# Performance work log

Measured on AMD Instinct MI355X. Metric: run time of the kernel, lower is better.

Reference implementation:

```python
import jax, jax.numpy as jnp
import numpy as np

LN_EPS = 1e-5

def _layernorm(x, g, b):
    mu = jnp.mean(x, axis=-1, keepdims=True)
    var = jnp.var(x, axis=-1, keepdims=True)
    return (x - mu) * jax.lax.rsqrt(var + LN_EPS) * g + b

def setup_inputs() -> dict:
    key = jax.random.key(0)
    B, S, D, H = 2, 2048, 1024, 16
    dh = D // H          # 64
    r = 48               # r_attn = int(0.75*min(D,dh))
    r_out = 768          # int(0.75*D)
    I = 4 * D            # GPT-2 MLP inner dim
    r_mlp = 512          # int(0.5*min(D,I))
    ks = jax.random.split(key, 24)
    sc = lambda *sh: 0.02
    inp = {
        'hidden_states': jax.random.normal(ks[0], (B, S, D), jnp.float32),
        'ln1_g': jnp.ones((D,), jnp.float32), 'ln1_b': jnp.zeros((D,), jnp.float32),
        'ln2_g': jnp.ones((D,), jnp.float32), 'ln2_b': jnp.zeros((D,), jnp.float32),
        'q_U': jax.random.normal(ks[1], (D, H, r), jnp.float32) * 0.02,
        'q_V': jax.random.normal(ks[2], (H, r, dh), jnp.float32) * 0.02,
        'q_b': jax.random.normal(ks[3], (H, dh), jnp.float32) * 0.02,
        'k_U': jax.random.normal(ks[4], (D, H, r), jnp.float32) * 0.02,
        'k_V': jax.random.normal(ks[5], (H, r, dh), jnp.float32) * 0.02,
        'k_b': jax.random.normal(ks[6], (H, dh), jnp.float32) * 0.02,
        'v_U': jax.random.normal(ks[7], (D, H, r), jnp.float32) * 0.02,
        'v_V': jax.random.normal(ks[8], (H, r, dh), jnp.float32) * 0.02,
        'v_b': jax.random.normal(ks[9], (H, dh), jnp.float32) * 0.02,
        'out_U': jax.random.normal(ks[10], (D, r_out), jnp.float32) * 0.02,
        'out_V': jax.random.normal(ks[11], (r_out, D), jnp.float32) * 0.02,
        'out_b': jnp.zeros((D,), jnp.float32),
        'fc1_U': jax.random.normal(ks[12], (D, r_mlp), jnp.float32) * 0.02,
        'fc1_V': jax.random.normal(ks[13], (r_mlp, I), jnp.float32) * 0.02,
        'fc1_b': jnp.zeros((I,), jnp.float32),
        'fc2_U': jax.random.normal(ks[14], (I, r_mlp), jnp.float32) * 0.02,
        'fc2_V': jax.random.normal(ks[15], (r_mlp, D), jnp.float32) * 0.02,
        'fc2_b': jnp.zeros((D,), jnp.float32),
    }
    return inp

def reference(hidden_states, ln1_g, ln1_b, ln2_g, ln2_b,
              q_U, q_V, q_b, k_U, k_V, k_b, v_U, v_V, v_b,
              out_U, out_V, out_b, fc1_U, fc1_V, fc1_b, fc2_U, fc2_V, fc2_b):
    B, S, D = hidden_states.shape
    H, dh = q_V.shape[0], q_V.shape[2]
    x = _layernorm(hidden_states, ln1_g, ln1_b)
    # low-rank per-head projections (latent P then reconstruct)
    Q = jnp.einsum('bsd,dhr,hre->bhse', x, q_U, q_V) + q_b[None, :, None, :]
    Pk = jnp.einsum('bsd,dhr->bhsr', x, k_U)
    Pv = jnp.einsum('bsd,dhr->bhsr', x, v_U)
    K = jnp.einsum('bhsr,hrd->bhsd', Pk, k_V) + k_b[None, :, None, :]
    V = jnp.einsum('bhsr,hrd->bhsd', Pv, v_V) + v_b[None, :, None, :]
    # causal scaled dot-product attention
    scale = 1.0 / jnp.sqrt(jnp.asarray(dh, x.dtype))
    scores = jnp.einsum('bhse,bhte->bhst', Q, K) * scale
    causal = jnp.tril(jnp.ones((S, S), bool))
    scores = jnp.where(causal[None, None], scores, jnp.asarray(-1e9, scores.dtype))
    attn = jax.nn.softmax(scores, axis=-1)
    ctx = jnp.einsum('bhst,bhtd->bhsd', attn, V)          # [B,H,S,dh]
    ctx = ctx.transpose(0, 2, 1, 3).reshape(B, S, D)
    attn_out = (ctx @ out_U) @ out_V + out_b
    h = hidden_states + attn_out
    # low-rank MLP with GPT-2 gelu (tanh approx)
    x2 = _layernorm(h, ln2_g, ln2_b)
    hmid = jax.nn.gelu((x2 @ fc1_U) @ fc1_V + fc1_b, approximate=True)
    mlp_out = (hmid @ fc2_U) @ fc2_V + fc2_b
    return h + mlp_out
```

## Files before the change

kernel.cpp:

```cpp
#include <hip/hip_runtime.h>
#include <hip/hip_bf16.h>

typedef float f32x4 __attribute__((ext_vector_type(4)));
typedef __bf16 bf16x8 __attribute__((ext_vector_type(8)));
typedef __bf16 bf16x4 __attribute__((ext_vector_type(4)));
typedef unsigned short u16x8 __attribute__((ext_vector_type(8)));
typedef unsigned short u16x4 __attribute__((ext_vector_type(4)));

#define QSCALE 0.180336881f

__device__ __forceinline__ unsigned short f2bf(float f) {
  union { float f; unsigned int u; } v; v.f = f;
  return (unsigned short)((v.u + 0x7FFFu + ((v.u >> 16) & 1u)) >> 16);
}

__device__ __forceinline__ f32x4 mfma16(bf16x8 a, bf16x8 b, f32x4 c) {
  return __builtin_amdgcn_mfma_f32_16x16x32_bf16(a, b, c, 0, 0, 0);
}

__device__ __forceinline__ void gload16(const unsigned short* g, unsigned short* l) {
  __builtin_amdgcn_global_load_lds(
      (const __attribute__((address_space(1))) void*)g,
      (__attribute__((address_space(3))) void*)l, 16, 0, 0);
}


__global__ void concat_bias_k(const float* __restrict__ qb, const float* __restrict__ kb,
                              const float* __restrict__ vb, float* __restrict__ out) {
  const int i = blockIdx.x * 256 + threadIdx.x;
  if (i >= 3072) return;
  const float* s = (i < 1024) ? qb : (i < 2048 ? kb : vb);
  out[i] = s[i & 1023] * (i < 1024 ? QSCALE : 1.0f);
}

__global__ void tcvt_k(const float* __restrict__ in, unsigned short* __restrict__ out,
                       int R, int C) {
  __shared__ float tile[32][33];
  const int x = blockIdx.x * 32 + threadIdx.x;
  const int y0 = blockIdx.y * 32;
#pragma unroll
  for (int i = 0; i < 32; i += 8)
    tile[threadIdx.y + i][threadIdx.x] = in[(size_t)(y0 + threadIdx.y + i) * C + x];
  __syncthreads();
  const int ox = y0 + threadIdx.x;
  const int oy0 = blockIdx.x * 32;
#pragma unroll
  for (int i = 0; i < 32; i += 8)
    out[(size_t)(oy0 + threadIdx.y + i) * R + ox] = f2bf(tile[threadIdx.x][threadIdx.y + i]);
}

__global__ void cvt_k(const float* __restrict__ in, unsigned short* __restrict__ out, int n) {
  const int i = (blockIdx.x * 256 + threadIdx.x) * 4;
  if (i >= n) return;
  const f32x4 v = *(const f32x4*)(in + i);
  u16x4 o;
#pragma unroll
  for (int k = 0; k < 4; ++k) o[k] = f2bf(v[k]);
  *(u16x4*)(out + i) = o;
}

__global__ void vtr_k(const unsigned short* __restrict__ QKV, unsigned short* __restrict__ VT) {
  __shared__ unsigned short tile[32][33];
  const int bh = blockIdx.z, b = bh >> 4, h = bh & 15;
  const int s0 = blockIdx.x * 32, d0 = blockIdx.y * 32;
  const unsigned short* src = QKV + (size_t)b * 2048 * 3072 + 2048 + h * 64;
#pragma unroll
  for (int i = 0; i < 32; i += 8)
    tile[threadIdx.y + i][threadIdx.x] = src[(size_t)(s0 + threadIdx.y + i) * 3072 + d0 + threadIdx.x];
  __syncthreads();
  unsigned short* dst = VT + (size_t)bh * 64 * 2048;
#pragma unroll
  for (int i = 0; i < 32; i += 8)
    dst[(size_t)(d0 + threadIdx.y + i) * 2048 + s0 + threadIdx.x] = tile[threadIdx.x][threadIdx.y + i];
}

__global__ __launch_bounds__(256) void wqkv_pre_k(
    const float* __restrict__ qU, const float* __restrict__ qV,
    const float* __restrict__ kU, const float* __restrict__ kV,
    const float* __restrict__ vU, const float* __restrict__ vV,
    unsigned short* __restrict__ WT) {
  __shared__ float Us[64][48];
  __shared__ float Vs[48][64];
  const int m = blockIdx.y >> 4, h = blockIdx.y & 15;
  const int d0 = blockIdx.x * 64;
  const float* U = (m == 0) ? qU : (m == 1 ? kU : vU);
  const float* V = (m == 0) ? qV : (m == 1 ? kV : vV);
  const float qs = (m == 0) ? QSCALE : 1.0f;
  const int t = threadIdx.x;
  for (int idx = t; idx < 64 * 48; idx += 256) {
    const int d = idx / 48, r = idx - d * 48;
    Us[d][r] = U[(size_t)(d0 + d) * 768 + h * 48 + r];
  }
  for (int idx = t; idx < 48 * 64; idx += 256) {
    const int r = idx >> 6, e = idx & 63;
    Vs[r][e] = V[(h * 48 + r) * 64 + e];
  }
  __syncthreads();
  const int e = t & 63, dg = t >> 6;
  for (int j = 0; j < 16; ++j) {
    const int d = dg * 16 + j;
    float s = 0.f;
#pragma unroll
    for (int r = 0; r < 48; ++r) s = fmaf(Us[d][r], Vs[r][e], s);
    WT[(size_t)(m * 1024 + h * 64 + e) * 1024 + d0 + d] = f2bf(s * qs);
  }
}

__global__ __launch_bounds__(256) void ln_k(
    const float* __restrict__ in, const float* __restrict__ gw,
    const float* __restrict__ bw, unsigned short* __restrict__ out) {
  const int row = blockIdx.x, t = threadIdx.x;
  const f32x4 v = *(const f32x4*)(in + (size_t)row * 1024 + t * 4);
  float s = v[0] + v[1] + v[2] + v[3];
  float ss = v[0] * v[0] + v[1] * v[1] + v[2] * v[2] + v[3] * v[3];
#pragma unroll
  for (int off = 1; off < 64; off <<= 1) {
    s += __shfl_xor(s, off);
    ss += __shfl_xor(ss, off);
  }
  __shared__ float red[8];
  if ((t & 63) == 0) { red[(t >> 6) * 2] = s; red[(t >> 6) * 2 + 1] = ss; }
  __syncthreads();
  s = red[0] + red[2] + red[4] + red[6];
  ss = red[1] + red[3] + red[5] + red[7];
  const float mean = s * (1.0f / 1024.0f);
  const float rstd = rsqrtf(ss * (1.0f / 1024.0f) - mean * mean + 1e-5f);
  const f32x4 g4 = *(const f32x4*)(gw + t * 4);
  const f32x4 b4 = *(const f32x4*)(bw + t * 4);
  u16x4 o;
#pragma unroll
  for (int i = 0; i < 4; ++i) o[i] = f2bf((v[i] - mean) * rstd * g4[i] + b4[i]);
  *(u16x4*)(out + (size_t)row * 1024 + t * 4) = o;
}

__device__ __forceinline__ void xcd_swz(int& bx, int& by, int nx, int ny) {
  const int nwg = nx * ny;
  if ((nwg & 7) == 0) {
    const int d = by * nx + bx;
    const int k = (d & 7) * (nwg >> 3) + (d >> 3);
    bx = k % nx;
    by = k / nx;
  }
}

template <int BM, int BN, int EPI, int OUTBF>
__global__ __launch_bounds__(256) void gemm_k(
    const unsigned short* __restrict__ A, const unsigned short* __restrict__ Bt,
    const float* __restrict__ bias, const float* __restrict__ resid,
    void* __restrict__ Cout, int M, int N, int K) {
  constexpr int MI = BM / 32;
  constexpr int FN = BN / 32;
  __shared__ unsigned short As[2][BM * 32];
  __shared__ unsigned short Bs[2][BN * 32];
  int bxi = blockIdx.x, byi = blockIdx.y;
  xcd_swz(bxi, byi, gridDim.x, gridDim.y);
  const int t = threadIdx.x;
  const int lane = t & 63, wid = t >> 6;
  const int m0 = byi * BM, n0 = bxi * BN;
  const int wm = (wid >> 1) * (BM / 2), wn = (wid & 1) * (BN / 2);
  const int fr = lane & 15, fg = (lane >> 4) * 8;

  f32x4 acc[MI][FN];
#pragma unroll
  for (int i = 0; i < MI; ++i)
#pragma unroll
    for (int j = 0; j < FN; ++j) acc[i][j] = (f32x4){0.f, 0.f, 0.f, 0.f};

  const unsigned short* Ag0 = A + (size_t)(m0 + (t >> 2)) * K + (t & 3) * 8;
  const unsigned short* Ag1 = A + (size_t)(m0 + 64 + (t >> 2)) * K + (t & 3) * 8;
  const unsigned short* Bg0 = Bt + (size_t)(n0 + (t >> 2)) * K + (t & 3) * 8;
  const unsigned short* Bg1 = Bt + (size_t)(n0 + 64 + (t >> 2)) * K + (t & 3) * 8;
  const int l0 = t * 8;

#define GEMM_STAGE(buf, ke)                                   \
  {                                                           \
    gload16(Ag0 + (ke), &As[buf][l0]);                        \
    if (BM == 128) gload16(Ag1 + (ke), &As[buf][l0 + 2048]);  \
    gload16(Bg0 + (ke), &Bs[buf][l0]);                        \
    if (BN == 128) gload16(Bg1 + (ke), &Bs[buf][l0 + 2048]);  \
  }

  const int nk = K >> 5;
  GEMM_STAGE(0, 0);

  for (int kt = 0; kt < nk; ++kt) {
    const int cur = kt & 1;
    __syncthreads();
    if (kt + 1 < nk) GEMM_STAGE(cur ^ 1, (kt + 1) * 32);
    bf16x8 af[MI], bfr[FN];
#pragma unroll
    for (int i = 0; i < MI; ++i) af[i] = *(const bf16x8*)&As[cur][(wm + i * 16 + fr) * 32 + fg];
#pragma unroll
    for (int j = 0; j < FN; ++j) bfr[j] = *(const bf16x8*)&Bs[cur][(wn + j * 16 + fr) * 32 + fg];
#pragma unroll
    for (int i = 0; i < MI; ++i)
#pragma unroll
      for (int j = 0; j < FN; ++j) acc[i][j] = mfma16(af[i], bfr[j], acc[i][j]);
  }
#undef GEMM_STAGE

#pragma unroll
  for (int j = 0; j < FN; ++j) {
    const int col = n0 + wn + j * 16 + fr;
    const float bval = (EPI >= 1) ? bias[col] : 0.0f;
#pragma unroll
    for (int i = 0; i < MI; ++i) {
#pragma unroll
      for (int r = 0; r < 4; ++r) {
        const int row = m0 + wm + i * 16 + ((lane >> 4) << 2) + r;
        float v = acc[i][j][r] + bval;
        if (EPI == 2) {
          const float z = 0.7978845608028654f * (v + 0.044715f * v * v * v);
          v = v - v / (__expf(2.0f * z) + 1.0f);
        }
        if (EPI == 3) v += resid[(size_t)row * N + col];
        if (OUTBF)
          ((unsigned short*)Cout)[(size_t)row * N + col] = f2bf(v);
        else
          ((float*)Cout)[(size_t)row * N + col] = v;
      }
    }
  }
}

__global__ __launch_bounds__(512) void attn_k(
    const unsigned short* __restrict__ QKV, const unsigned short* __restrict__ VT,
    unsigned short* __restrict__ ctx) {
  __shared__ unsigned short Ks[2][64 * 64];
  __shared__ unsigned short Vs[2][64 * 64];
  __shared__ unsigned short Ps[8][16 * 64];
  int bxi = blockIdx.x, byi = blockIdx.y;
  xcd_swz(bxi, byi, 16, 32);
  const int qi = ((byi >> 1) & 1) ? (15 - bxi) : bxi;
  const int bh = byi, b = bh >> 4, h = bh & 15;
  const int nt = 2 * qi + 2;
  const int q0b = qi * 128;
  const int t = threadIdx.x, lane = t & 63, w = t >> 6;
  const int g = lane >> 4, c = lane & 15;
  const int cks = c & 7;
  const size_t base = (size_t)b * 2048 * 3072;

  const int r0 = t >> 3, ch0 = t & 7;
  const int lw = r0 * 64 + ((ch0 ^ (r0 & 7)) * 8);
  const unsigned short* Kg = QKV + base + 1024 + h * 64 + (size_t)r0 * 3072 + ch0 * 8;
  const unsigned short* Vg = VT + ((size_t)bh * 64 + r0) * 2048 + ch0 * 8;

  const int kro0 = (g ^ cks) * 8, kro1 = ((4 + g) ^ cks) * 8;

  bf16x8 onef;
#pragma unroll
  for (int i = 0; i < 8; ++i) onef[i] = (__bf16)1.0f;

  const int qrow = q0b + w * 16 + c;
  const unsigned short* qp = QKV + base + (size_t)qrow * 3072 + h * 64 + g * 8;
  const bf16x8 qf0 = *(const bf16x8*)qp;
  const bf16x8 qf1 = *(const bf16x8*)(qp + 32);

  f32x4 o[4];
#pragma unroll
  for (int d = 0; d < 4; ++d) o[d] = (f32x4){0.f, 0.f, 0.f, 0.f};
  f32x4 ol = (f32x4){0.f, 0.f, 0.f, 0.f};
  float mrow = -1e30f;

  u16x8 kr, vr;
#define ATTN_LOAD(kt_)                                        \
  {                                                           \
    kr = *(const u16x8*)(Kg + (size_t)(kt_) * 64 * 3072);     \
    vr = *(const u16x8*)(Vg + (kt_) * 64);                    \
  }
#define ATTN_WRITE(buf)                                       \
  {                                                           \
    *(u16x8*)&Ks[buf][lw] = kr;                               \
    *(u16x8*)&Vs[buf][lw] = vr;                               \
  }

  ATTN_LOAD(0);
  ATTN_WRITE(0);
  if (nt > 1) ATTN_LOAD(1);
  __syncthreads();

  const int fsrc = g * 20;

  for (int j = 0; j < nt; ++j) {
    const int cur = j & 1;
    const int kbase = j * 64;
    const bool active = (kbase <= q0b + w * 16 + 15);

    if (active) {
      f32x4 s4[4];
      __builtin_amdgcn_s_setprio(1);
#pragma unroll
      for (int t16 = 0; t16 < 4; ++t16) {
        const int krow = (t16 * 16 + c) * 64;
        const bf16x8 kf0 = *(const bf16x8*)&Ks[cur][krow + kro0];
        const bf16x8 kf1 = *(const bf16x8*)&Ks[cur][krow + kro1];
        f32x4 a = (f32x4){0.f, 0.f, 0.f, 0.f};
        a = mfma16(kf0, qf0, a);
        a = mfma16(kf1, qf1, a);
        s4[t16] = a;
      }
      __builtin_amdgcn_s_setprio(0);
      if (kbase + 63 > qrow) {
#pragma unroll
        for (int t16 = 0; t16 < 4; ++t16)
#pragma unroll
          for (int r = 0; r < 4; ++r)
            if (kbase + t16 * 16 + 4 * g + r > qrow) s4[t16][r] = -1e30f;
      }
      float mx = s4[0][0];
#pragma unroll
      for (int t16 = 0; t16 < 4; ++t16)
#pragma unroll
        for (int r = 0; r < 4; ++r) mx = fmaxf(mx, s4[t16][r]);
      mx = fmaxf(mx, __shfl_xor(mx, 16));
      mx = fmaxf(mx, __shfl_xor(mx, 32));
      const float mn = fmaxf(mrow, mx);
      const float fac = exp2f(mrow - mn);
      mrow = mn;
#pragma unroll
      for (int t16 = 0; t16 < 4; ++t16) {
        bf16x4 pw;
#pragma unroll
        for (int r = 0; r < 4; ++r) pw[r] = (__bf16)exp2f(s4[t16][r] - mrow);
        *(bf16x4*)&Ps[w][c * 64 + (((2 * t16 + (g >> 1)) ^ cks) * 8) + (g & 1) * 4] = pw;
      }
      float fo[4];
#pragma unroll
      for (int r = 0; r < 4; ++r) fo[r] = __shfl(fac, fsrc + r);
#pragma unroll
      for (int d = 0; d < 4; ++d)
#pragma unroll
        for (int r = 0; r < 4; ++r) o[d][r] *= fo[r];
#pragma unroll
      for (int r = 0; r < 4; ++r) ol[r] *= fo[r];
      __builtin_amdgcn_s_setprio(1);
#pragma unroll
      for (int ks = 0; ks < 2; ++ks) {
        const int po = ((ks * 4 + g) ^ cks) * 8;
        const bf16x8 pf = *(const bf16x8*)&Ps[w][c * 64 + po];
#pragma unroll
        for (int d = 0; d < 4; ++d) {
          const bf16x8 vf = *(const bf16x8*)&Vs[cur][(d * 16 + c) * 64 + po];
          o[d] = mfma16(pf, vf, o[d]);
        }
        ol = mfma16(pf, onef, ol);
      }
      __builtin_amdgcn_s_setprio(0);
    }

    if (j + 1 < nt) {
      __syncthreads();
      ATTN_WRITE(cur ^ 1);
      if (j + 2 < nt) ATTN_LOAD(j + 2);
      __syncthreads();
    }
  }
#pragma unroll
  for (int d = 0; d < 4; ++d)
#pragma unroll
    for (int r = 0; r < 4; ++r) {
      const float v = o[d][r] / ol[r];
      ctx[(size_t)(b * 2048 + q0b + w * 16 + g * 4 + r) * 1024 + h * 64 + d * 16 + c] = f2bf(v);
    }
#undef ATTN_LOAD
#undef ATTN_WRITE
}


extern "C" void kernel_launch(void* const* d_in, const int* in_sizes, int n_in,
                              void* d_out, int out_size, void* d_ws, size_t ws_size,
                              hipStream_t stream) {
  const float* hidden = (const float*)d_in[0];
  const float* ln1g = (const float*)d_in[1];
  const float* ln1b = (const float*)d_in[2];
  const float* ln2g = (const float*)d_in[3];
  const float* ln2b = (const float*)d_in[4];
  const float* qU = (const float*)d_in[5];
  const float* qV = (const float*)d_in[6];
  const float* qb = (const float*)d_in[7];
  const float* kU = (const float*)d_in[8];
  const float* kV = (const float*)d_in[9];
  const float* kb = (const float*)d_in[10];
  const float* vU = (const float*)d_in[11];
  const float* vV = (const float*)d_in[12];
  const float* vb = (const float*)d_in[13];
  const float* outU = (const float*)d_in[14];
  const float* outV = (const float*)d_in[15];
  const float* outb = (const float*)d_in[16];
  const float* fc1U = (const float*)d_in[17];
  const float* fc1V = (const float*)d_in[18];
  const float* fc1b = (const float*)d_in[19];
  const float* fc2U = (const float*)d_in[20];
  const float* fc2V = (const float*)d_in[21];
  const float* fc2b = (const float*)d_in[22];
  float* out = (float*)d_out;

  char* p = (char*)d_ws;
  unsigned short* x1x2 = (unsigned short*)p; p += (size_t)4096 * 1024 * 2;
  unsigned short* WqT_t1 = (unsigned short*)p; p += (size_t)3072 * 1024 * 2;
  float* bqkv = (float*)p; p += 3072 * 4;
  char* bigA = p; p += (size_t)4096 * 3072 * 2 + (size_t)4096 * 1024 * 2;
  unsigned short* QKV = (unsigned short*)bigA;
  unsigned short* ctxb = (unsigned short*)(bigA + (size_t)4096 * 3072 * 2);
  unsigned short* hmid = (unsigned short*)bigA;
  char* wo = p; p += (size_t)1024 * 768 * 2 * 2 + (size_t)1024 * 1024 * 2;
  unsigned short* outUb = (unsigned short*)wo;
  unsigned short* outVT = (unsigned short*)(wo + (size_t)1024 * 768 * 2);
  unsigned short* WoutT = (unsigned short*)(wo + (size_t)1024 * 768 * 2 * 2);
  unsigned short* t2 = (unsigned short*)wo;
  float* hbuf = (float*)p; p += (size_t)4096 * 1024 * 4;
  unsigned short* VT = (unsigned short*)hbuf;
  unsigned short* fc1UT = (unsigned short*)p; p += (size_t)512 * 1024 * 2;
  unsigned short* fc1VT = (unsigned short*)p; p += (size_t)4096 * 512 * 2;
  unsigned short* fc2UT = (unsigned short*)p; p += (size_t)512 * 4096 * 2;
  unsigned short* fc2VT = (unsigned short*)p; p += (size_t)1024 * 512 * 2;

  const dim3 b256(256);
  const dim3 tb(32, 8);

  concat_bias_k<<<12, b256, 0, stream>>>(qb, kb, vb, bqkv);
  wqkv_pre_k<<<dim3(16, 48), b256, 0, stream>>>(qU, qV, kU, kV, vU, vV, WqT_t1);
  tcvt_k<<<dim3(32, 24), tb, 0, stream>>>(outV, outVT, 768, 1024);
  cvt_k<<<768, b256, 0, stream>>>(outU, outUb, 1024 * 768);
  tcvt_k<<<dim3(16, 32), tb, 0, stream>>>(fc1U, fc1UT, 1024, 512);
  tcvt_k<<<dim3(128, 16), tb, 0, stream>>>(fc1V, fc1VT, 512, 4096);
  tcvt_k<<<dim3(16, 128), tb, 0, stream>>>(fc2U, fc2UT, 4096, 512);
  tcvt_k<<<dim3(32, 16), tb, 0, stream>>>(fc2V, fc2VT, 512, 1024);

  ln_k<<<4096, b256, 0, stream>>>(hidden, ln1g, ln1b, x1x2);
  gemm_k<128, 128, 1, 1><<<dim3(24, 32), b256, 0, stream>>>(x1x2, WqT_t1, bqkv, nullptr, QKV, 4096, 3072, 1024);
  vtr_k<<<dim3(64, 2, 32), tb, 0, stream>>>(QKV, VT);
  gemm_k<128, 128, 0, 1><<<dim3(8, 8), b256, 0, stream>>>(outVT, outUb, nullptr, nullptr, WoutT, 1024, 1024, 768);
  attn_k<<<dim3(16, 32), dim3(512), 0, stream>>>(QKV, VT, ctxb);
  gemm_k<64, 128, 3, 0><<<dim3(8, 64), b256, 0, stream>>>(ctxb, WoutT, outb, hidden, hbuf, 4096, 1024, 1024);

  ln_k<<<4096, b256, 0, stream>>>(hbuf, ln2g, ln2b, x1x2);
  gemm_k<64, 64, 0, 1><<<dim3(8, 64), b256, 0, stream>>>(x1x2, fc1UT, nullptr, nullptr, WqT_t1, 4096, 512, 1024);
  gemm_k<128, 128, 2, 1><<<dim3(32, 32), b256, 0, stream>>>(WqT_t1, fc1VT, fc1b, nullptr, hmid, 4096, 4096, 512);
  gemm_k<64, 64, 0, 1><<<dim3(8, 64), b256, 0, stream>>>(hmid, fc2UT, nullptr, nullptr, t2, 4096, 512, 4096);
  gemm_k<64, 128, 3, 0><<<dim3(8, 64), b256, 0, stream>>>(t2, fc2VT, fc2b, hbuf, out, 4096, 1024, 512);
}
```

Before: 291.4 us.

## Triple-buffer GEMM k-loop with vmcnt waits and stage bf16 epilogue through LDS

Moves the GEMM main loop from double to triple buffering. It prefetches two stages ahead and uses explicit s_waitcnt vmcnt plus a raw barrier instead of __syncthreads, so global loads overlap more with MFMA work. For bf16 outputs, each wave writes its results into a padded LDS tile and then stores 16-byte vectors per row, replacing scattered 2-byte global stores. The cost is more LDS per block, which may lower occupancy, and the hand-tuned wait counts depend on how many loads each stage issues.

```diff
diff --git a/kernel.cpp b/kernel.cpp
--- a/kernel.cpp
+++ b/kernel.cpp
@@ -150,8 +150,13 @@
     void* __restrict__ Cout, int M, int N, int K) {
   constexpr int MI = BM / 32;
   constexpr int FN = BN / 32;
-  __shared__ unsigned short As[2][BM * 32];
-  __shared__ unsigned short Bs[2][BN * 32];
+  constexpr int NL = (BM == 128 ? 2 : 1) + (BN == 128 ? 2 : 1);
+  constexpr int SM_KLOOP = 3 * (BM + BN) * 32;
+  constexpr int SM_EPI = OUTBF ? 4 * (BM / 2) * 72 : 0;
+  constexpr int SME = SM_KLOOP > SM_EPI ? SM_KLOOP : SM_EPI;
+  __shared__ unsigned short smem[SME];
+  unsigned short* As = smem;
+  unsigned short* Bs = smem + 3 * BM * 32;
   int bxi = blockIdx.x, byi = blockIdx.y;
   xcd_swz(bxi, byi, gridDim.x, gridDim.y);
   const int t = threadIdx.x;
@@ -172,52 +177,89 @@
   const unsigned short* Bg1 = Bt + (size_t)(n0 + 64 + (t >> 2)) * K + (t & 3) * 8;
   const int l0 = t * 8;
 
-#define GEMM_STAGE(buf, ke)                                   \
-  {                                                           \
-    gload16(Ag0 + (ke), &As[buf][l0]);                        \
-    if (BM == 128) gload16(Ag1 + (ke), &As[buf][l0 + 2048]);  \
-    gload16(Bg0 + (ke), &Bs[buf][l0]);                        \
-    if (BN == 128) gload16(Bg1 + (ke), &Bs[buf][l0 + 2048]);  \
+#define GEMM_STAGE(buf, ke)                                             \
+  {                                                                     \
+    gload16(Ag0 + (ke), &As[(buf) * BM * 32 + l0]);                     \
+    if (BM == 128) gload16(Ag1 + (ke), &As[(buf) * BM * 32 + l0 + 2048]); \
+    gload16(Bg0 + (ke), &Bs[(buf) * BN * 32 + l0]);                     \
+    if (BN == 128) gload16(Bg1 + (ke), &Bs[(buf) * BN * 32 + l0 + 2048]); \
   }
 
   const int nk = K >> 5;
   GEMM_STAGE(0, 0);
-
+  if (nk > 1) GEMM_STAGE(1, 32);
+
+  int cur = 0, sb = 2;
   for (int kt = 0; kt < nk; ++kt) {
-    const int cur = kt & 1;
+    if (kt + 1 < nk)
+      asm volatile("s_waitcnt vmcnt(%0)" ::"n"(NL) : "memory");
+    else
+      asm volatile("s_waitcnt vmcnt(0)" ::: "memory");
+    __builtin_amdgcn_s_barrier();
+    __builtin_amdgcn_sched_barrier(0);
+    if (kt + 2 < nk) GEMM_STAGE(sb, (kt + 2) * 32);
+    bf16x8 af[MI], bfr[FN];
+#pragma unroll
+    for (int i = 0; i < MI; ++i)
+      af[i] = *(const bf16x8*)&As[cur * BM * 32 + (wm + i * 16 + fr) * 32 + fg];
+#pragma unroll
+    for (int j = 0; j < FN; ++j)
+      bfr[j] = *(const bf16x8*)&Bs[cur * BN * 32 + (wn + j * 16 + fr) * 32 + fg];
+#pragma unroll
+    for (int i = 0; i < MI; ++i)
+#pragma unroll
+      for (int j = 0; j < FN; ++j) acc[i][j] = mfma16(af[i], bfr[j], acc[i][j]);
+    cur = (cur == 2) ? 0 : cur + 1;
+    sb = (sb == 2) ? 0 : sb + 1;
+  }
+#undef GEMM_STAGE
+
+  if (OUTBF) {
     __syncthreads();
-    if (kt + 1 < nk) GEMM_STAGE(cur ^ 1, (kt + 1) * 32);
-    bf16x8 af[MI], bfr[FN];
-#pragma unroll
-    for (int i = 0; i < MI; ++i) af[i] = *(const bf16x8*)&As[cur][(wm + i * 16 + fr) * 32 + fg];
-#pragma unroll
-    for (int j = 0; j < FN; ++j) bfr[j] = *(const bf16x8*)&Bs[cur][(wn + j * 16 + fr) * 32 + fg];
-#pragma unroll
-    for (int i = 0; i < MI; ++i)
-#pragma unroll
-      for (int j = 0; j < FN; ++j) acc[i][j] = mfma16(af[i], bfr[j], acc[i][j]);
-  }
-#undef GEMM_STAGE
-
-#pragma unroll
-  for (int j = 0; j < FN; ++j) {
-    const int col = n0 + wn + j * 16 + fr;
-    const float bval = (EPI >= 1) ? bias[col] : 0.0f;
-#pragma unroll
-    for (int i = 0; i < MI; ++i) {
-#pragma unroll
-      for (int r = 0; r < 4; ++r) {
-        const int row = m0 + wm + i * 16 + ((lane >> 4) << 2) + r;
-        float v = acc[i][j][r] + bval;
-        if (EPI == 2) {
-          const float z = 0.7978845608028654f * (v + 0.044715f * v * v * v);
-          v = v - v / (__expf(2.0f * z) + 1.0f);
+    unsigned short* eb = smem + wid * ((BM / 2) * 72);
+#pragma unroll
+    for (int j = 0; j < FN; ++j) {
+      const int colL = j * 16 + fr;
+      const float bval = (EPI >= 1) ? bias[n0 + wn + colL] : 0.0f;
+#pragma unroll
+      for (int i = 0; i < MI; ++i) {
+#pragma unroll
+        for (int r = 0; r < 4; ++r) {
+          const int rl = i * 16 + ((lane >> 4) << 2) + r;
+          float v = acc[i][j][r] + bval;
+          if (EPI == 2) {
+            const float z = 0.7978845608028654f * (v + 0.044715f * v * v * v);
+            v = v - v / (__expf(2.0f * z) + 1.0f);
+          }
+          eb[rl * 72 + colL] = f2bf(v);
         }
-        if (EPI == 3) v += resid[(size_t)row * N + col];
-        if (OUTBF)
-          ((unsigned short*)Cout)[(size_t)row * N + col] = f2bf(v);
-        else
+      }
+    }
+    __builtin_amdgcn_s_barrier();
+    constexpr int CH = (BN / 2) / 8;
+    constexpr int RPI = 64 / CH;
+    const int c2 = lane % CH, r2b = lane / CH;
+    unsigned short* Cg = (unsigned short*)Cout;
+#pragma unroll
+    for (int it = 0; it < (BM / 2) / RPI; ++it) {
+      const int r2 = r2b + it * RPI;
+      const u16x8 vv = *(const u16x8*)&eb[r2 * 72 + c2 * 8];
+      *(u16x8*)&Cg[(size_t)(m0 + wm + r2) * N + n0 + wn + c2 * 8] = vv;
+    }
+  } else {
+#pragma unroll
+    for (int j = 0; j < FN; ++j) {
+      const int col = n0 + wn + j * 16 + fr;
+      const float bval = (EPI >= 1) ? bias[col] : 0.0f;
+#pragma unroll
+      for (int i = 0; i < MI; ++i) {
+#pragma unroll
+        for (int r = 0; r < 4; ++r) {
+          const int row = m0 + wm + i * 16 + ((lane >> 4) << 2) + r;
+          float v = acc[i][j][r] + bval;
+          if (EPI == 3) v += resid[(size_t)row * N + col];
           ((float*)Cout)[(size_t)row * N + col] = v;
+        }
       }
     }
   }
```

Measured after the change: 258.8 us. 11.2% less time.
